# Kernel tuning notes

Hardware: AMD Instinct MI355X
Metric: run time of the kernel (lower is better)

The kernel has to match this reference:

```python
import jax, jax.numpy as jnp
import numpy as np

Q_DIM = 2048
HEADS = 16
HEAD_DIM = 128
INNER = HEADS * HEAD_DIM          # 2048
MLP_HID = int(Q_DIM * 4.0)        # 8192
MLP_MULT = 2
EPS = 1e-05
B, S = 2, 2048


def setup_inputs() -> dict:
    key = jax.random.key(0)
    ks = jax.random.split(key, 4)
    hidden_states = jax.random.normal(ks[0], (B, S, Q_DIM), dtype=jnp.float32)
    # interleaved RoPE tables: cos/sin of shape [S, HEAD_DIM]
    half = HEAD_DIM // 2
    freqs = 1.0 / (10000.0 ** (np.arange(half, dtype=np.float64) / half))
    ang = np.outer(np.arange(S, dtype=np.float64), freqs)      # [S, half]
    ang = np.repeat(ang, 2, axis=-1)                            # [S, HEAD_DIM]
    rope_cos = jnp.asarray(np.cos(ang), dtype=jnp.float32)
    rope_sin = jnp.asarray(np.sin(ang), dtype=jnp.float32)
    fused_out = 3 * INNER + MLP_HID * MLP_MULT                  # 22528
    W_qkv_mlp = jax.random.normal(ks[1], (Q_DIM, fused_out), dtype=jnp.float32) * (Q_DIM ** -0.5)
    norm_q_w = jnp.ones((HEAD_DIM,), dtype=jnp.float32)
    norm_k_w = jnp.ones((HEAD_DIM,), dtype=jnp.float32)
    W_out = jax.random.normal(ks[2], (INNER + MLP_HID, Q_DIM), dtype=jnp.float32) * ((INNER + MLP_HID) ** -0.5)
    b_out = jnp.zeros((Q_DIM,), dtype=jnp.float32)
    return {"hidden_states": hidden_states, "rope_cos": rope_cos, "rope_sin": rope_sin,
            "W_qkv_mlp": W_qkv_mlp, "norm_q_w": norm_q_w, "norm_k_w": norm_k_w,
            "W_out": W_out, "b_out": b_out}


def _rms_norm(x, w):
    # RMSNorm over the last (head_dim) axis
    return x * jax.lax.rsqrt(jnp.mean(x * x, axis=-1, keepdims=True) + EPS) * w


def _apply_rope(x, cos, sin):
    # x: [B, S, H, D]; interleaved rotate-half (diffusers real-rope convention)
    xr = x.reshape(*x.shape[:-1], HEAD_DIM // 2, 2)
    rot = jnp.stack([-xr[..., 1], xr[..., 0]], axis=-1).reshape(x.shape)
    return x * cos[None, :, None, :] + rot * sin[None, :, None, :]


def reference(hidden_states, rope_cos, rope_sin, W_qkv_mlp, norm_q_w, norm_k_w, W_out, b_out):
    b, s, _ = hidden_states.shape
    proj = hidden_states @ W_qkv_mlp                              # [B,S,22528]
    qkv, mlp_h = jnp.split(proj, [3 * INNER], axis=-1)
    q, k, v = jnp.split(qkv, 3, axis=-1)
    q = q.reshape(b, s, HEADS, HEAD_DIM)
    k = k.reshape(b, s, HEADS, HEAD_DIM)
    v = v.reshape(b, s, HEADS, HEAD_DIM)
    q = _rms_norm(q, norm_q_w)
    k = _rms_norm(k, norm_k_w)
    q = _apply_rope(q, rope_cos, rope_sin)
    k = _apply_rope(k, rope_cos, rope_sin)
    scale = HEAD_DIM ** -0.5
    scores = jnp.einsum('bqhd,bkhd->bhqk', q, k) * scale          # [B,H,S,S]
    attn = jax.nn.softmax(scores, axis=-1)
    out_attn = jnp.einsum('bhqk,bkhd->bqhd', attn, v).reshape(b, s, INNER)
    m1, m2 = jnp.split(mlp_h, 2, axis=-1)                         # SwiGLU
    mlp_out = jax.nn.silu(m1) * m2                                # [B,S,MLP_HID]
    cat = jnp.concatenate([out_attn, mlp_out], axis=-1)           # [B,S,INNER+MLP_HID]
    return cat @ W_out + b_out
```

## Files before the change

kernel.cpp:

```cpp
#include <hip/hip_runtime.h>

typedef unsigned short u16;
typedef unsigned int u32;
typedef __bf16 bf16x8 __attribute__((ext_vector_type(8)));
typedef float f32x4 __attribute__((ext_vector_type(4)));

#define MFMA16(a, b, c) __builtin_amdgcn_mfma_f32_16x16x32_bf16((a), (b), (c), 0, 0, 0)

#define S_LEN 2048
#define D_HEAD 128
#define NHEADS 16
#define NBH 32
#define QDIM 2048
#define NPROJ 22528
#define NCAT 10240
#define MROWS 4096

#define BARRIER() __builtin_amdgcn_s_barrier()
#define WAITVM0() asm volatile("s_waitcnt vmcnt(0)" ::: "memory")

__device__ __forceinline__ float bf2f(u16 u) { return __uint_as_float(((u32)u) << 16); }
__device__ __forceinline__ u16 f2bf(float f) {
  u32 u = __float_as_uint(f);
  return (u16)((u + 0x7FFFu + ((u >> 16) & 1u)) >> 16);
}
__device__ __forceinline__ void gld16(const void* g, void* l) {
  __builtin_amdgcn_global_load_lds((__attribute__((address_space(1))) void*)(g),
                                   (__attribute__((address_space(3))) void*)(l), 16, 0, 0);
}

__global__ __launch_bounds__(256) void f32_to_bf16(const float* __restrict__ in,
                                                   u16* __restrict__ out) {
  const u32 i = blockIdx.x * 256 + threadIdx.x;
  const float4 v = ((const float4*)in)[i];
  uint2 o;
  o.x = (u32)f2bf(v.x) | ((u32)f2bf(v.y) << 16);
  o.y = (u32)f2bf(v.z) | ((u32)f2bf(v.w) << 16);
  ((uint2*)out)[i] = o;
}

__global__ __launch_bounds__(256) void transpose_f32_bf16(const float* __restrict__ in,
                                                          u16* __restrict__ out, int R, int C) {
  __shared__ u16 tile[64][65];
  const int tx = threadIdx.x & 63;
  const int ty = threadIdx.x >> 6;
  const int c0 = blockIdx.x * 64;
  const int r0 = blockIdx.y * 64;
#pragma unroll
  for (int it = 0; it < 16; ++it) {
    const int rr = ty * 16 + it;
    tile[rr][tx] = f2bf(in[(size_t)(r0 + rr) * C + c0 + tx]);
  }
  __syncthreads();
#pragma unroll
  for (int it = 0; it < 16; ++it) {
    const int rr = ty * 16 + it;
    out[(size_t)(c0 + rr) * R + r0 + tx] = tile[tx][rr];
  }
}

__global__ __launch_bounds__(256) void transpose_bf16_b(const u16* __restrict__ in,
                                                        u16* __restrict__ out, int R, int C) {
  __shared__ u16 tile[64][65];
  const int z = blockIdx.z;
  in += (size_t)z * R * C;
  out += (size_t)z * R * C;
  const int tx = threadIdx.x & 63;
  const int ty = threadIdx.x >> 6;
  const int c0 = blockIdx.x * 64;
  const int r0 = blockIdx.y * 64;
#pragma unroll
  for (int it = 0; it < 16; ++it) {
    const int rr = ty * 16 + it;
    tile[rr][tx] = in[(size_t)(r0 + rr) * C + c0 + tx];
  }
  __syncthreads();
#pragma unroll
  for (int it = 0; it < 16; ++it) {
    const int rr = ty * 16 + it;
    out[(size_t)(c0 + rr) * R + r0 + tx] = tile[tx][rr];
  }
}

template <int OUTF32, int COLMAJ>
__global__ __launch_bounds__(256, 2) void gemm_bt(const u16* __restrict__ A,
                                                  const u16* __restrict__ Bt,
                                                  void* __restrict__ Cvoid,
                                                  const float* __restrict__ bias, int N, int K,
                                                  int nb) {
  __shared__ u16 As[128 * 64];
  __shared__ u16 Bs[128 * 64];
  const int t = threadIdx.x;
  const int l = t & 63;
  const int w = t >> 6;
  const int lr = l & 15;
  const int lg = l >> 4;
  const int nwg = gridDim.x;
  const int cpx = nwg >> 3;
  const int swz = (blockIdx.x & 7) * cpx + (blockIdx.x >> 3);
  const int bm = COLMAJ ? (swz % nb) : (swz / nb);
  const int bn = COLMAJ ? (swz / nb) : (swz % nb);
  const int m0 = bm * 128;
  const int n0 = bn * 128;
  const int wm = (w >> 1) * 64;
  const int wn = (w & 1) * 64;

  f32x4 acc[4][4] = {};
  const int obase = w * 1024 + l * 16;

  for (int k0 = 0; k0 < K; k0 += 64) {
#pragma unroll
    for (int rnd = 0; rnd < 4; ++rnd) {
      const int o = obase + rnd * 4096;
      const int row = o >> 7;
      const int g = (o & 127) >> 4;
      const int gs = g ^ (row & 7);
      gld16(A + (size_t)(m0 + row) * K + k0 + gs * 8, &As[rnd * 2048 + w * 512]);
      gld16(Bt + (size_t)(n0 + row) * K + k0 + gs * 8, &Bs[rnd * 2048 + w * 512]);
    }
    __syncthreads();

    bf16x8 af[4][2], bfr[4][2];
#pragma unroll
    for (int i = 0; i < 4; ++i) {
#pragma unroll
      for (int kc = 0; kc < 2; ++kc) {
        const int ra = wm + i * 16 + lr;
        af[i][kc] = *(const bf16x8*)&As[ra * 64 + (((kc * 4 + lg) ^ (ra & 7)) * 8)];
        const int rb = wn + i * 16 + lr;
        bfr[i][kc] = *(const bf16x8*)&Bs[rb * 64 + (((kc * 4 + lg) ^ (rb & 7)) * 8)];
      }
    }
#pragma unroll
    for (int kc = 0; kc < 2; ++kc)
#pragma unroll
      for (int i = 0; i < 4; ++i)
#pragma unroll
        for (int j = 0; j < 4; ++j)
          acc[i][j] = MFMA16(af[i][kc], bfr[j][kc], acc[i][j]);
    __syncthreads();
  }

  if (OUTF32) {
    float* C = (float*)Cvoid;
#pragma unroll
    for (int i = 0; i < 4; ++i)
#pragma unroll
      for (int j = 0; j < 4; ++j)
#pragma unroll
        for (int r = 0; r < 4; ++r) {
          const int row = m0 + wm + i * 16 + lg * 4 + r;
          const int col = n0 + wn + j * 16 + lr;
          C[(size_t)row * N + col] = acc[i][j][r] + bias[col];
        }
  } else {
    u16* C = (u16*)Cvoid;
#pragma unroll
    for (int i = 0; i < 4; ++i)
#pragma unroll
      for (int j = 0; j < 4; ++j)
#pragma unroll
        for (int r = 0; r < 4; ++r) {
          const int row = m0 + wm + i * 16 + lg * 4 + r;
          const int col = n0 + wn + j * 16 + lr;
          C[(size_t)row * N + col] = f2bf(acc[i][j][r]);
        }
  }
}

__global__ __launch_bounds__(256) void norm_rope(const u16* __restrict__ proj,
                                                 const float* __restrict__ cosT,
                                                 const float* __restrict__ sinT,
                                                 const float* __restrict__ wq,
                                                 const float* __restrict__ wk,
                                                 u16* __restrict__ Qb, u16* __restrict__ Kb,
                                                 u16* __restrict__ Vb) {
  const int l = threadIdx.x & 63;
  const int wg = blockIdx.x * 4 + (threadIdx.x >> 6);
  const int h = wg & 15;
  const int r = wg >> 4;
  const int b = r >> 11;
  const int s = r & 2047;
  const int bh = (b << 4) + h;

  const u16* p = proj + (size_t)r * NPROJ + h * 128 + 2 * l;
  const u32 qu = *(const u32*)(p);
  const u32 ku = *(const u32*)(p + QDIM);
  const u32 vu = *(const u32*)(p + 2 * QDIM);

  const float q0 = bf2f(qu & 0xffff), q1 = bf2f(qu >> 16);
  const float k0 = bf2f(ku & 0xffff), k1 = bf2f(ku >> 16);

  float sq = q0 * q0 + q1 * q1;
  float sk = k0 * k0 + k1 * k1;
#pragma unroll
  for (int m = 1; m < 64; m <<= 1) {
    sq += __shfl_xor(sq, m);
    sk += __shfl_xor(sk, m);
  }
  const float scq = rsqrtf(sq * (1.0f / 128.0f) + 1e-5f);
  const float sck = rsqrtf(sk * (1.0f / 128.0f) + 1e-5f);

  const float2 cc = *(const float2*)&cosT[s * 128 + 2 * l];
  const float2 ssn = *(const float2*)&sinT[s * 128 + 2 * l];
  const float w0 = wq[2 * l], w1 = wq[2 * l + 1];
  const float x0 = wk[2 * l], x1 = wk[2 * l + 1];

  const float qn0 = q0 * scq * w0, qn1 = q1 * scq * w1;
  const float kn0 = k0 * sck * x0, kn1 = k1 * sck * x1;

  const float ATT = 0.08838834764831845f;
  const float qr0 = (qn0 * cc.x - qn1 * ssn.x) * ATT;
  const float qr1 = (qn1 * cc.y + qn0 * ssn.y) * ATT;
  const float kr0 = kn0 * cc.x - kn1 * ssn.x;
  const float kr1 = kn1 * cc.y + kn0 * ssn.y;

  const size_t dst = ((size_t)bh * S_LEN + s) * 128 + 2 * l;
  *(u32*)(Qb + dst) = (u32)f2bf(qr0) | ((u32)f2bf(qr1) << 16);
  *(u32*)(Kb + dst) = (u32)f2bf(kr0) | ((u32)f2bf(kr1) << 16);
  *(u32*)(Vb + dst) = vu;
}

__global__ __launch_bounds__(256) void swiglu(const u16* __restrict__ proj,
                                              u16* __restrict__ Cat) {
  const u32 i = blockIdx.x * 256 + threadIdx.x;
  const u32 r = i >> 11;
  const u32 c = (i & 2047) * 4;
  const u16* p1 = proj + (size_t)r * NPROJ + 3 * QDIM + c;
  const uint2 a = *(const uint2*)p1;
  const uint2 bv = *(const uint2*)(p1 + 8192);
  const float a0 = bf2f(a.x & 0xffff), a1 = bf2f(a.x >> 16);
  const float a2 = bf2f(a.y & 0xffff), a3 = bf2f(a.y >> 16);
  const float b0 = bf2f(bv.x & 0xffff), b1 = bf2f(bv.x >> 16);
  const float b2 = bf2f(bv.y & 0xffff), b3 = bf2f(bv.y >> 16);
  const float o0 = a0 / (1.f + __expf(-a0)) * b0;
  const float o1 = a1 / (1.f + __expf(-a1)) * b1;
  const float o2 = a2 / (1.f + __expf(-a2)) * b2;
  const float o3 = a3 / (1.f + __expf(-a3)) * b3;
  uint2 o;
  o.x = (u32)f2bf(o0) | ((u32)f2bf(o1) << 16);
  o.y = (u32)f2bf(o2) | ((u32)f2bf(o3) << 16);
  *(uint2*)(Cat + (size_t)r * NCAT + QDIM + c) = o;
}

__global__ __launch_bounds__(256, 2) void attn_fwd(const u16* __restrict__ Qb,
                                                   const u16* __restrict__ Kb,
                                                   const u16* __restrict__ Vt,
                                                   u16* __restrict__ Cat) {
  __shared__ u16 Ks[2][64 * 128];
  __shared__ u16 Vs[2][128 * 64];
  __shared__ u16 Ps[4][32 * 64];

  const int t = threadIdx.x;
  const int l = t & 63;
  const int w = t >> 6;
  const int lr = l & 15;
  const int lg = l >> 4;
  const int qt = blockIdx.x;
  const int bh = blockIdx.y;
  const int b = bh >> 4;
  const int h = bh & 15;
  const int q0 = qt * 128 + w * 32;
  const int obase = w * 1024 + l * 16;

  const size_t kbase = (size_t)bh * S_LEN * 128;
  const size_t vbase = (size_t)bh * 128 * S_LEN;

  bf16x8 qf[2][4];
#pragma unroll
  for (int im = 0; im < 2; ++im)
#pragma unroll
    for (int kc = 0; kc < 4; ++kc)
      qf[im][kc] =
          *(const bf16x8*)&Qb[((size_t)bh * S_LEN + q0 + im * 16 + lr) * 128 + kc * 32 + lg * 8];

  f32x4 oacc[2][8] = {};
  float mrun[2][4], lrun[2][4];
#pragma unroll
  for (int im = 0; im < 2; ++im)
#pragma unroll
    for (int r = 0; r < 4; ++r) {
      mrun[im][r] = -1e30f;
      lrun[im][r] = 0.f;
    }

  u16* P = Ps[w];

  auto stageKV = [&](int buf, int kt2) {
    const int kk0 = kt2 * 64;
#pragma unroll
    for (int rnd = 0; rnd < 4; ++rnd) {
      const int o = obase + rnd * 4096;
      {
        const int key = o >> 8;
        const int g = (o & 255) >> 4;
        const int gs = g ^ (key & 7);
        gld16(Kb + kbase + (size_t)(kk0 + key) * 128 + gs * 8,
              &Ks[buf][rnd * 2048 + w * 512]);
      }
      {
        const int d = o >> 7;
        const int g = (o & 127) >> 4;
        const int gs = g ^ (d & 7);
        gld16(Vt + vbase + (size_t)d * S_LEN + kk0 + gs * 8,
              &Vs[buf][rnd * 2048 + w * 512]);
      }
    }
  };

  stageKV(0, 0);
  WAITVM0();
  BARRIER();

  int cur = 0;
  for (int kt = 0; kt < 32; ++kt) {
    if (kt + 1 < 32) stageKV(cur ^ 1, kt + 1);

    const u16* Kc = &Ks[cur][0];
    const u16* Vc = &Vs[cur][0];

    f32x4 sf[2][4] = {};
    __builtin_amdgcn_s_setprio(1);
#pragma unroll
    for (int j = 0; j < 4; ++j) {
      const int kr = j * 16 + lr;
      bf16x8 kf[4];
#pragma unroll
      for (int kc = 0; kc < 4; ++kc)
        kf[kc] = *(const bf16x8*)&Kc[kr * 128 + (((kc * 4 + lg) ^ (kr & 7)) * 8)];
#pragma unroll
      for (int kc = 0; kc < 4; ++kc)
#pragma unroll
        for (int im = 0; im < 2; ++im)
          sf[im][j] = MFMA16(qf[im][kc], kf[kc], sf[im][j]);
    }
    __builtin_amdgcn_s_setprio(0);

#pragma unroll
    for (int im = 0; im < 2; ++im) {
#pragma unroll
      for (int r = 0; r < 4; ++r) {
        float v = fmaxf(fmaxf(sf[im][0][r], sf[im][1][r]), fmaxf(sf[im][2][r], sf[im][3][r]));
        v = fmaxf(v, __shfl_xor(v, 1));
        v = fmaxf(v, __shfl_xor(v, 2));
        v = fmaxf(v, __shfl_xor(v, 4));
        v = fmaxf(v, __shfl_xor(v, 8));
        const float mnew = fmaxf(mrun[im][r], v);
        const float alpha = __expf(mrun[im][r] - mnew);
        mrun[im][r] = mnew;
        float psum = 0.f;
#pragma unroll
        for (int j = 0; j < 4; ++j) {
          const float pv = __expf(sf[im][j][r] - mnew);
          sf[im][j][r] = pv;
          psum += pv;
        }
        psum += __shfl_xor(psum, 1);
        psum += __shfl_xor(psum, 2);
        psum += __shfl_xor(psum, 4);
        psum += __shfl_xor(psum, 8);
        lrun[im][r] = lrun[im][r] * alpha + psum;
#pragma unroll
        for (int df = 0; df < 8; ++df) oacc[im][df][r] *= alpha;
      }
    }

#pragma unroll
    for (int im = 0; im < 2; ++im)
#pragma unroll
      for (int j = 0; j < 4; ++j)
#pragma unroll
        for (int r = 0; r < 4; ++r) {
          const int q = im * 16 + lg * 4 + r;
          const int key = j * 16 + lr;
          const int g = key >> 3;
          P[q * 64 + ((g ^ (q & 7)) * 8) + (key & 7)] = f2bf(sf[im][j][r]);
        }

    __builtin_amdgcn_s_setprio(1);
#pragma unroll
    for (int kc = 0; kc < 2; ++kc) {
      bf16x8 pa[2];
#pragma unroll
      for (int im = 0; im < 2; ++im) {
        const int q = im * 16 + lr;
        pa[im] = *(const bf16x8*)&P[q * 64 + (((kc * 4 + lg) ^ (q & 7)) * 8)];
      }
#pragma unroll
      for (int df = 0; df < 8; ++df) {
        const int d = df * 16 + lr;
        const bf16x8 vb = *(const bf16x8*)&Vc[d * 64 + (((kc * 4 + lg) ^ (d & 7)) * 8)];
#pragma unroll
        for (int im = 0; im < 2; ++im) oacc[im][df] = MFMA16(pa[im], vb, oacc[im][df]);
      }
    }
    __builtin_amdgcn_s_setprio(0);

    WAITVM0();
    BARRIER();
    cur ^= 1;
  }

#pragma unroll
  for (int im = 0; im < 2; ++im)
#pragma unroll
    for (int r = 0; r < 4; ++r) {
      const float inv = 1.0f / lrun[im][r];
      const int row = b * S_LEN + q0 + im * 16 + lg * 4 + r;
#pragma unroll
      for (int df = 0; df < 8; ++df) {
        const int col = h * 128 + df * 16 + lr;
        Cat[(size_t)row * NCAT + col] = f2bf(oacc[im][df][r] * inv);
      }
    }
}

extern "C" void kernel_launch(void* const* d_in, const int* in_sizes, int n_in, void* d_out,
                              int out_size, void* d_ws, size_t ws_size, hipStream_t stream) {
  (void)in_sizes; (void)n_in; (void)out_size; (void)ws_size;
  const float* hs = (const float*)d_in[0];
  const float* rcos = (const float*)d_in[1];
  const float* rsin = (const float*)d_in[2];
  const float* Wqkv = (const float*)d_in[3];
  const float* wq = (const float*)d_in[4];
  const float* wk = (const float*)d_in[5];
  const float* Wout = (const float*)d_in[6];
  const float* bout = (const float*)d_in[7];
  float* out = (float*)d_out;

  char* ws = (char*)d_ws;
  size_t off = 0;
  auto nxt = [&](size_t bytes) {
    char* p = ws + off;
    off += (bytes + 255) & ~(size_t)255;
    return p;
  };
  u16* Xb = (u16*)nxt((size_t)MROWS * QDIM * 2);
  u16* Wqkvt = (u16*)nxt((size_t)NPROJ * QDIM * 2);
  u16* Woutt = (u16*)nxt((size_t)QDIM * NCAT * 2);
  u16* proj = (u16*)nxt((size_t)MROWS * NPROJ * 2);
  u16* Qb = (u16*)nxt((size_t)NBH * S_LEN * D_HEAD * 2);
  u16* Kb = (u16*)nxt((size_t)NBH * S_LEN * D_HEAD * 2);
  u16* Vb = (u16*)nxt((size_t)NBH * S_LEN * D_HEAD * 2);
  u16* Vt = (u16*)nxt((size_t)NBH * S_LEN * D_HEAD * 2);
  u16* Cat = (u16*)nxt((size_t)MROWS * NCAT * 2);

  f32_to_bf16<<<(MROWS * QDIM / 4) / 256, 256, 0, stream>>>(hs, Xb);
  transpose_f32_bf16<<<dim3(NPROJ / 64, QDIM / 64), 256, 0, stream>>>(Wqkv, Wqkvt, QDIM, NPROJ);
  transpose_f32_bf16<<<dim3(QDIM / 64, NCAT / 64), 256, 0, stream>>>(Wout, Woutt, NCAT, QDIM);

  gemm_bt<0, 1><<<(MROWS / 128) * (NPROJ / 128), 256, 0, stream>>>(Xb, Wqkvt, proj, nullptr,
                                                                   NPROJ, QDIM, MROWS / 128);

  norm_rope<<<MROWS * NHEADS / 4, 256, 0, stream>>>(proj, rcos, rsin, wq, wk, Qb, Kb, Vb);
  transpose_bf16_b<<<dim3(D_HEAD / 64, S_LEN / 64, NBH), 256, 0, stream>>>(Vb, Vt, S_LEN, D_HEAD);

  swiglu<<<(MROWS * 8192 / 4) / 256, 256, 0, stream>>>(proj, Cat);

  attn_fwd<<<dim3(S_LEN / 128, NBH), 256, 0, stream>>>(Qb, Kb, Vt, Cat);

  gemm_bt<1, 0><<<(MROWS / 128) * (QDIM / 128), 256, 0, stream>>>(Cat, Woutt, out, bout, QDIM,
                                                                  NCAT, QDIM / 128);
}
```

Before: 933.7 us.

## Fuse SwiGLU into projection GEMM epilogue via interleaved weight layout

The transposed MLP weight rows are interleaved in 16-column groups so each GEMM output tile holds matching gate and up columns. A new GEMM epilogue mode computes silu(a1)*a2 and writes bf16 straight into the concat buffer, which removes the standalone swiglu kernel and the write and read of the 4096x16384 MLP half of proj. The projection is split into a QKV GEMM and an MLP GEMM. The block-index swizzle for L2 locality is dropped in favour of a plain 2D grid, which may cost some cache reuse.

```diff
diff --git a/kernel.cpp b/kernel.cpp
--- a/kernel.cpp
+++ b/kernel.cpp
@@ -13,6 +13,8 @@
 #define NBH 32
 #define QDIM 2048
 #define NPROJ 22528
+#define NQKV 6144
+#define NMLP 16384
 #define NCAT 10240
 #define MROWS 4096
 
@@ -39,6 +41,7 @@
   ((uint2*)out)[i] = o;
 }
 
+template <int REMAP>
 __global__ __launch_bounds__(256) void transpose_f32_bf16(const float* __restrict__ in,
                                                           u16* __restrict__ out, int R, int C) {
   __shared__ u16 tile[64][65];
@@ -55,7 +58,14 @@
 #pragma unroll
   for (int it = 0; it < 16; ++it) {
     const int rr = ty * 16 + it;
-    out[(size_t)(c0 + rr) * R + r0 + tx] = tile[tx][rr];
+    int orow = c0 + rr;
+    if (REMAP && orow >= NQKV) {
+      const int c = orow - NQKV;
+      const int f = c & 8191;
+      const int sel = c >> 13;
+      orow = NQKV + (((f >> 4) << 5) | (sel << 4) | (f & 15));
+    }
+    out[(size_t)orow * R + r0 + tx] = tile[tx][rr];
   }
 }
 
@@ -82,12 +92,11 @@
   }
 }
 
-template <int OUTF32, int COLMAJ>
+template <int OUTMODE>
 __global__ __launch_bounds__(256, 2) void gemm_bt(const u16* __restrict__ A,
                                                   const u16* __restrict__ Bt,
                                                   void* __restrict__ Cvoid,
-                                                  const float* __restrict__ bias, int N, int K,
-                                                  int nb) {
+                                                  const float* __restrict__ bias, int N, int K) {
   __shared__ u16 As[128 * 64];
   __shared__ u16 Bs[128 * 64];
   const int t = threadIdx.x;
@@ -95,13 +104,8 @@
   const int w = t >> 6;
   const int lr = l & 15;
   const int lg = l >> 4;
-  const int nwg = gridDim.x;
-  const int cpx = nwg >> 3;
-  const int swz = (blockIdx.x & 7) * cpx + (blockIdx.x >> 3);
-  const int bm = COLMAJ ? (swz % nb) : (swz / nb);
-  const int bn = COLMAJ ? (swz / nb) : (swz % nb);
-  const int m0 = bm * 128;
-  const int n0 = bn * 128;
+  const int m0 = blockIdx.y * 128;
+  const int n0 = blockIdx.x * 128;
   const int wm = (w >> 1) * 64;
   const int wn = (w & 1) * 64;
 
@@ -141,7 +145,7 @@
     __syncthreads();
   }
 
-  if (OUTF32) {
+  if (OUTMODE == 1) {
     float* C = (float*)Cvoid;
 #pragma unroll
     for (int i = 0; i < 4; ++i)
@@ -153,7 +157,7 @@
           const int col = n0 + wn + j * 16 + lr;
           C[(size_t)row * N + col] = acc[i][j][r] + bias[col];
         }
-  } else {
+  } else if (OUTMODE == 0) {
     u16* C = (u16*)Cvoid;
 #pragma unroll
     for (int i = 0; i < 4; ++i)
@@ -164,6 +168,21 @@
           const int row = m0 + wm + i * 16 + lg * 4 + r;
           const int col = n0 + wn + j * 16 + lr;
           C[(size_t)row * N + col] = f2bf(acc[i][j][r]);
+        }
+  } else {
+    u16* C = (u16*)Cvoid;
+#pragma unroll
+    for (int i = 0; i < 4; ++i)
+#pragma unroll
+      for (int jj = 0; jj < 2; ++jj)
+#pragma unroll
+        for (int r = 0; r < 4; ++r) {
+          const int row = m0 + wm + i * 16 + lg * 4 + r;
+          const float a1 = acc[i][2 * jj][r];
+          const float a2 = acc[i][2 * jj + 1][r];
+          const float fz = a1 / (1.f + __expf(-a1)) * a2;
+          const int col = ((n0 + wn) >> 1) + jj * 16 + lr;
+          C[(size_t)row * N + col] = f2bf(fz);
         }
   }
 }
@@ -183,7 +202,7 @@
   const int s = r & 2047;
   const int bh = (b << 4) + h;
 
-  const u16* p = proj + (size_t)r * NPROJ + h * 128 + 2 * l;
+  const u16* p = proj + (size_t)r * NQKV + h * 128 + 2 * l;
   const u32 qu = *(const u32*)(p);
   const u32 ku = *(const u32*)(p + QDIM);
   const u32 vu = *(const u32*)(p + 2 * QDIM);
@@ -219,28 +238,6 @@
   *(u32*)(Qb + dst) = (u32)f2bf(qr0) | ((u32)f2bf(qr1) << 16);
   *(u32*)(Kb + dst) = (u32)f2bf(kr0) | ((u32)f2bf(kr1) << 16);
   *(u32*)(Vb + dst) = vu;
-}
-
-__global__ __launch_bounds__(256) void swiglu(const u16* __restrict__ proj,
-                                              u16* __restrict__ Cat) {
-  const u32 i = blockIdx.x * 256 + threadIdx.x;
-  const u32 r = i >> 11;
-  const u32 c = (i & 2047) * 4;
-  const u16* p1 = proj + (size_t)r * NPROJ + 3 * QDIM + c;
-  const uint2 a = *(const uint2*)p1;
-  const uint2 bv = *(const uint2*)(p1 + 8192);
-  const float a0 = bf2f(a.x & 0xffff), a1 = bf2f(a.x >> 16);
-  const float a2 = bf2f(a.y & 0xffff), a3 = bf2f(a.y >> 16);
-  const float b0 = bf2f(bv.x & 0xffff), b1 = bf2f(bv.x >> 16);
-  const float b2 = bf2f(bv.y & 0xffff), b3 = bf2f(bv.y >> 16);
-  const float o0 = a0 / (1.f + __expf(-a0)) * b0;
-  const float o1 = a1 / (1.f + __expf(-a1)) * b1;
-  const float o2 = a2 / (1.f + __expf(-a2)) * b2;
-  const float o3 = a3 / (1.f + __expf(-a3)) * b3;
-  uint2 o;
-  o.x = (u32)f2bf(o0) | ((u32)f2bf(o1) << 16);
-  o.y = (u32)f2bf(o2) | ((u32)f2bf(o3) << 16);
-  *(uint2*)(Cat + (size_t)r * NCAT + QDIM + c) = o;
 }
 
 __global__ __launch_bounds__(256, 2) void attn_fwd(const u16* __restrict__ Qb,
@@ -438,7 +435,7 @@
   u16* Xb = (u16*)nxt((size_t)MROWS * QDIM * 2);
   u16* Wqkvt = (u16*)nxt((size_t)NPROJ * QDIM * 2);
   u16* Woutt = (u16*)nxt((size_t)QDIM * NCAT * 2);
-  u16* proj = (u16*)nxt((size_t)MROWS * NPROJ * 2);
+  u16* proj = (u16*)nxt((size_t)MROWS * NQKV * 2);
   u16* Qb = (u16*)nxt((size_t)NBH * S_LEN * D_HEAD * 2);
   u16* Kb = (u16*)nxt((size_t)NBH * S_LEN * D_HEAD * 2);
   u16* Vb = (u16*)nxt((size_t)NBH * S_LEN * D_HEAD * 2);
@@ -446,19 +443,20 @@
   u16* Cat = (u16*)nxt((size_t)MROWS * NCAT * 2);
 
   f32_to_bf16<<<(MROWS * QDIM / 4) / 256, 256, 0, stream>>>(hs, Xb);
-  transpose_f32_bf16<<<dim3(NPROJ / 64, QDIM / 64), 256, 0, stream>>>(Wqkv, Wqkvt, QDIM, NPROJ);
-  transpose_f32_bf16<<<dim3(QDIM / 64, NCAT / 64), 256, 0, stream>>>(Wout, Woutt, NCAT, QDIM);
-
-  gemm_bt<0, 1><<<(MROWS / 128) * (NPROJ / 128), 256, 0, stream>>>(Xb, Wqkvt, proj, nullptr,
-                                                                   NPROJ, QDIM, MROWS / 128);
+  transpose_f32_bf16<1><<<dim3(NPROJ / 64, QDIM / 64), 256, 0, stream>>>(Wqkv, Wqkvt, QDIM,
+                                                                         NPROJ);
+  transpose_f32_bf16<0><<<dim3(QDIM / 64, NCAT / 64), 256, 0, stream>>>(Wout, Woutt, NCAT, QDIM);
+
+  gemm_bt<0><<<dim3(NQKV / 128, MROWS / 128), 256, 0, stream>>>(Xb, Wqkvt, proj, nullptr,
+                                                                NQKV, QDIM);
+  gemm_bt<2><<<dim3(NMLP / 128, MROWS / 128), 256, 0, stream>>>(
+      Xb, Wqkvt + (size_t)NQKV * QDIM, Cat + QDIM, nullptr, NCAT, QDIM);
 
   norm_rope<<<MROWS * NHEADS / 4, 256, 0, stream>>>(proj, rcos, rsin, wq, wk, Qb, Kb, Vb);
   transpose_bf16_b<<<dim3(D_HEAD / 64, S_LEN / 64, NBH), 256, 0, stream>>>(Vb, Vt, S_LEN, D_HEAD);
 
-  swiglu<<<(MROWS * 8192 / 4) / 256, 256, 0, stream>>>(proj, Cat);
-
   attn_fwd<<<dim3(S_LEN / 128, NBH), 256, 0, stream>>>(Qb, Kb, Vt, Cat);
 
-  gemm_bt<1, 0><<<(MROWS / 128) * (QDIM / 128), 256, 0, stream>>>(Cat, Woutt, out, bout, QDIM,
-                                                                  NCAT, QDIM / 128);
-}
+  gemm_bt<1><<<dim3(QDIM / 128, MROWS / 128), 256, 0, stream>>>(Cat, Woutt, out, bout, QDIM,
+                                                                NCAT);
+}
```

After: 816.6 us. 1.14x faster.
